# Optimization experiments

Measured on AMD Instinct MI355X. Metric: run time of the kernel, lower is better.

Reference implementation:

```python
import jax, jax.numpy as jnp
import numpy as np

D = 1024      # d_model
H = 16        # num_heads
HW = D // H   # head_width = 64
FF = 4 * D    # hidden_dim = 4096
BATCH = 2
T = 2048
EPS = 1e-5


def layer_norm(x, g, b):
    mu = jnp.mean(x, axis=-1, keepdims=True)
    var = jnp.mean(jnp.square(x - mu), axis=-1, keepdims=True)
    return (x - mu) * jax.lax.rsqrt(var + EPS) * g + b


def setup_inputs() -> dict:
    key = jax.random.key(0)
    ks = jax.random.split(key, 7)
    s = 0.02
    return {
        "x": jax.random.normal(ks[0], (BATCH, T, D), dtype=jnp.float32),
        "Wq": jax.random.normal(ks[1], (D, D), dtype=jnp.float32) * s,
        "Wk": jax.random.normal(ks[2], (D, D), dtype=jnp.float32) * s,
        "Wv": jax.random.normal(ks[3], (D, D), dtype=jnp.float32) * s,
        "W1": jax.random.normal(ks[4], (FF, D), dtype=jnp.float32) * s,
        "W2": jax.random.normal(ks[5], (D, FF), dtype=jnp.float32) * s,
        "g1": jnp.ones((D,), dtype=jnp.float32),
        "b1": jnp.zeros((D,), dtype=jnp.float32),
        "g2": jnp.ones((D,), dtype=jnp.float32),
        "b2": jnp.zeros((D,), dtype=jnp.float32),
    }


def reference(x, Wq, Wk, Wv, W1, W2, g1, b1, g2, b2):
    N, t, d = x.shape
    # norm1
    xn = layer_norm(x, g1, b1)

    # --- MHSA with ALiBi + causal mask (math mirrors torch module) ---
    def heads(y):  # (N,t,D) -> (N,H,t,HW)
        return y.reshape(N, t, H, HW).transpose(0, 2, 1, 3)

    q = heads(xn @ Wq.T)
    k = heads(xn @ Wk.T)
    v = heads(xn @ Wv.T)

    scores = jnp.einsum("nhqd,nhkd->nhqk", q, k) / np.sqrt(HW).astype(np.float32)

    pos = jnp.arange(t)
    rel = (pos[None, :] - pos[:, None]).astype(x.dtype)           # [t,t], rel[i,j]=j-i
    slopes = (2.0 ** (-(jnp.arange(1, H + 1)) * (8.0 / H))).astype(x.dtype)  # [H]
    alibi = slopes[:, None, None] * rel                            # [H,t,t]
    causal = jnp.where(pos[None, :] > pos[:, None],
                       jnp.array(-jnp.inf, x.dtype),
                       jnp.array(0.0, x.dtype))                    # [t,t]

    att = jax.nn.softmax(scores + alibi[None] + causal[None, None], axis=-1)
    o = jnp.einsum("nhqk,nhkd->nhqd", att, v)
    o = o.transpose(0, 2, 1, 3).reshape(N, t, d)

    att_out = xn + o

    # --- MLP: Linear -> SiLU -> Linear ---
    h = layer_norm(att_out, g2, b2)
    m = jax.nn.silu(h @ W1.T) @ W2.T
    return att_out + m
```

## Files before the change

kernel.cpp:

```cpp
#include <hip/hip_runtime.h>

#define DMODEL 1024
#define NHEAD  16
#define HWID   64
#define FFDIM  4096
#define NBATCH 2
#define SEQT   2048
#define NTOK   4096
#define QKLD   3072

using bf8    = __attribute__((ext_vector_type(8))) short;
using f32x4  = __attribute__((ext_vector_type(4))) float;
using f32x16 = __attribute__((ext_vector_type(16))) float;

__device__ inline short to_bf16(float f) {
  unsigned u = __float_as_uint(f);
  return (short)((u + 0x7fffu + ((u >> 16) & 1u)) >> 16);
}
__device__ inline float from_bf16(short s) {
  return __uint_as_float(((unsigned)(unsigned short)s) << 16);
}
__device__ inline float exp2_fast(float x) {
  float r;
  asm("v_exp_f32 %0, %1" : "=v"(r) : "v"(x));
  return r;
}
__device__ inline unsigned cvt_pk_bf16(float lo, float hi) {
  unsigned r;
  asm("v_cvt_pk_bf16_f32 %0, %1, %2" : "=v"(r) : "v"(lo), "v"(hi));
  return r;
}
__device__ inline void lds_load16(const void* g, void* l) {
  __builtin_amdgcn_global_load_lds(
      (const __attribute__((address_space(1))) void*)g,
      (__attribute__((address_space(3))) void*)l, 16, 0, 0);
}

__global__ __launch_bounds__(256)
void prep_kernel(const float* __restrict__ Wq, const float* __restrict__ Wk,
                 const float* __restrict__ Wv, const float* __restrict__ W1,
                 const float* __restrict__ W2, short* __restrict__ wqkv,
                 short* __restrict__ w1b, short* __restrict__ w2b,
                 const float* __restrict__ x, const float* __restrict__ g1,
                 const float* __restrict__ b1, short* __restrict__ xn) {
  __shared__ float red[8];
  if (blockIdx.x < 11264) {
    int i = blockIdx.x * 256 + threadIdx.x;
    const float* src;
    short* dst;
    if (i < 1048576)      { src = W1; dst = w1b; }
    else if (i < 2097152) { src = W2; dst = w2b;            i -= 1048576; }
    else if (i < 2359296) { src = Wq; dst = wqkv;           i -= 2097152; }
    else if (i < 2621440) { src = Wk; dst = wqkv + 1048576; i -= 2359296; }
    else                  { src = Wv; dst = wqkv + 2097152; i -= 2621440; }
    float4 v = ((const float4*)src)[i];
    short4 o;
    o.x = to_bf16(v.x); o.y = to_bf16(v.y);
    o.z = to_bf16(v.z); o.w = to_bf16(v.w);
    ((short4*)dst)[i] = o;
  } else {
    const int row = blockIdx.x - 11264;
    const int t = threadIdx.x;
    const float4 v = ((const float4*)(x + (long)row * DMODEL))[t];
    float s  = v.x + v.y + v.z + v.w;
    float s2 = v.x * v.x + v.y * v.y + v.z * v.z + v.w * v.w;
#pragma unroll
    for (int m = 1; m < 64; m <<= 1) {
      s  += __shfl_xor(s, m);
      s2 += __shfl_xor(s2, m);
    }
    if ((t & 63) == 0) { red[t >> 6] = s; red[4 + (t >> 6)] = s2; }
    __syncthreads();
    s  = red[0] + red[1] + red[2] + red[3];
    s2 = red[4] + red[5] + red[6] + red[7];
    const float mu = s * (1.f / DMODEL);
    const float rs = rsqrtf(s2 * (1.f / DMODEL) - mu * mu + 1e-5f);
    const float4 gv = ((const float4*)g1)[t];
    const float4 bv = ((const float4*)b1)[t];
    short4 o;
    o.x = to_bf16((v.x - mu) * rs * gv.x + bv.x);
    o.y = to_bf16((v.y - mu) * rs * gv.y + bv.y);
    o.z = to_bf16((v.z - mu) * rs * gv.z + bv.z);
    o.w = to_bf16((v.w - mu) * rs * gv.w + bv.w);
    ((short4*)(xn + (long)row * DMODEL))[t] = o;
  }
}

__global__ __launch_bounds__(256)
void ln_kernel(const float* __restrict__ x, const float* __restrict__ g,
               const float* __restrict__ b, short* __restrict__ out) {
  const int row = blockIdx.x;
  const int t = threadIdx.x;
  const float4 v = ((const float4*)(x + (long)row * DMODEL))[t];
  float s  = v.x + v.y + v.z + v.w;
  float s2 = v.x * v.x + v.y * v.y + v.z * v.z + v.w * v.w;
#pragma unroll
  for (int m = 1; m < 64; m <<= 1) {
    s  += __shfl_xor(s, m);
    s2 += __shfl_xor(s2, m);
  }
  __shared__ float red[8];
  if ((t & 63) == 0) { red[t >> 6] = s; red[4 + (t >> 6)] = s2; }
  __syncthreads();
  s  = red[0] + red[1] + red[2] + red[3];
  s2 = red[4] + red[5] + red[6] + red[7];
  const float mu = s * (1.f / DMODEL);
  const float rs = rsqrtf(s2 * (1.f / DMODEL) - mu * mu + 1e-5f);
  const float4 gv = ((const float4*)g)[t];
  const float4 bv = ((const float4*)b)[t];
  short4 o;
  o.x = to_bf16((v.x - mu) * rs * gv.x + bv.x);
  o.y = to_bf16((v.y - mu) * rs * gv.y + bv.y);
  o.z = to_bf16((v.z - mu) * rs * gv.z + bv.z);
  o.w = to_bf16((v.w - mu) * rs * gv.w + bv.w);
  ((short4*)(out + (long)row * DMODEL))[t] = o;
}

template <int EPI, int NF>
__global__ __launch_bounds__(512, 2)
void gemm256(const short* __restrict__ A, const short* __restrict__ Bw,
             void* __restrict__ Cout, int N, int lda, int ldb, int Kslice,
             long zstride) {
  __shared__ short lds[2][2][16384];
  const int tid = threadIdx.x;
  const int wid = tid >> 6, lane = tid & 63;
  const int l15 = lane & 15, l4 = lane >> 4;
  const int wm = wid >> 2, wn = wid & 3;
  const int BROWS = NF * 64;

  const int gx = gridDim.x, nwg = gx * gridDim.y;
  const int wg = blockIdx.y * gx + blockIdx.x;
  const int sw = (wg & 7) * (nwg >> 3) + (wg >> 3);
  const int sx = gx >> 2;
  const int st = sw >> 4, w16 = sw & 15;
  const long bm = (long)((st / sx) * 4 + (w16 >> 2)) * 256;
  const long bn = (long)((st % sx) * 4 + (w16 & 3)) * BROWS;
  const long kofs = (long)blockIdx.z * Kslice;
  const int NT = Kslice >> 6;

  long arow[2], brow[2];
  int  sgel[2], dofs[2];
#pragma unroll
  for (int l = 0; l < 2; ++l) {
    const int g = l * 512 + tid;
    const int row = g >> 2;
    sgel[l] = ((g & 3) ^ ((row >> 1) & 3)) * 8;
    dofs[l] = g * 16;
    arow[l] = (bm + row) * (long)lda + kofs;
    const int rb = (row < BROWS) ? row : (BROWS - 1);
    brow[l] = (bn + rb) * (long)ldb + kofs;
  }
  auto stage_half = [&](int h) {
    if (h >= (NT << 2)) return;
    const int th = h >> 2, hi = h & 3, buf = th & 1;
    const int ks = hi >> 1, isA = hi & 1;
    char* db = (char*)&lds[buf][isA ? 0 : 1][0] + ks * 16384;
    const long kb = (long)th * 64 + ks * 32;
#pragma unroll
    for (int l = 0; l < 2; ++l) {
      const short* src = (isA ? A + arow[l] : Bw + brow[l]) + kb + sgel[l];
      lds_load16(src, db + dofs[l]);
    }
  };

  const int xsw = (l4 ^ ((l15 >> 1) & 3)) << 4;
  const int aofs = (wm * 128 + l15) * 64 + xsw;
  const int bofs = (wn * (NF * 16) + l15) * 64 + xsw;

  f32x4 acc[8][NF] = {};
  bf8 fa[4], fa2[4], fb[NF];

#define PH_MID                                             \
  __builtin_amdgcn_s_barrier();                            \
  __builtin_amdgcn_s_setprio(1);
#define PH_END                                             \
  __builtin_amdgcn_s_setprio(0);                           \
  __builtin_amdgcn_s_barrier();                            \
  asm volatile("" ::: "memory");

#pragma unroll
  for (int h = 0; h < 7; ++h) stage_half(h);
  asm volatile("s_waitcnt vmcnt(6)" ::: "memory");
  __builtin_amdgcn_s_barrier();
  asm volatile("" ::: "memory");

  for (int u = 0; u < NT; ++u) {
    const int buf = u & 1;
    const char* pa = (const char*)&lds[buf][0][0];
    const char* pb = (const char*)&lds[buf][1][0];
#pragma unroll
    for (int m = 0; m < 4; ++m) fa[m] = *(const bf8*)(pa + aofs + m * 1024);
#pragma unroll
    for (int n = 0; n < NF; ++n) fb[n] = *(const bf8*)(pb + bofs + n * 1024);
    stage_half(4 * u + 7);
    PH_MID
#pragma unroll
    for (int m = 0; m < 4; ++m)
#pragma unroll
      for (int n = 0; n < NF; ++n)
        acc[m][n] = __builtin_amdgcn_mfma_f32_16x16x32_bf16(fa[m], fb[n], acc[m][n], 0, 0, 0);
    PH_END
#pragma unroll
    for (int m = 0; m < 4; ++m) fa2[m] = *(const bf8*)(pa + aofs + (4 + m) * 1024);
    stage_half(4 * u + 8);
    PH_MID
#pragma unroll
    for (int m = 0; m < 4; ++m)
#pragma unroll
      for (int n = 0; n < NF; ++n)
        acc[4 + m][n] = __builtin_amdgcn_mfma_f32_16x16x32_bf16(fa2[m], fb[n], acc[4 + m][n], 0, 0, 0);
    PH_END
#pragma unroll
    for (int m = 0; m < 4; ++m) fa[m] = *(const bf8*)(pa + 16384 + aofs + m * 1024);
#pragma unroll
    for (int n = 0; n < NF; ++n) fb[n] = *(const bf8*)(pb + 16384 + bofs + n * 1024);
    stage_half(4 * u + 9);
    PH_MID
#pragma unroll
    for (int m = 0; m < 4; ++m)
#pragma unroll
      for (int n = 0; n < NF; ++n)
        acc[m][n] = __builtin_amdgcn_mfma_f32_16x16x32_bf16(fa[m], fb[n], acc[m][n], 0, 0, 0);
    PH_END
#pragma unroll
    for (int m = 0; m < 4; ++m) fa2[m] = *(const bf8*)(pa + 16384 + aofs + (4 + m) * 1024);
    stage_half(4 * u + 10);
    if (u <= NT - 3)      asm volatile("s_waitcnt vmcnt(6)" ::: "memory");
    else if (u == NT - 2) asm volatile("s_waitcnt vmcnt(0)" ::: "memory");
    PH_MID
#pragma unroll
    for (int m = 0; m < 4; ++m)
#pragma unroll
      for (int n = 0; n < NF; ++n)
        acc[4 + m][n] = __builtin_amdgcn_mfma_f32_16x16x32_bf16(fa2[m], fb[n], acc[4 + m][n], 0, 0, 0);
    PH_END
  }
#undef PH_MID
#undef PH_END

#pragma unroll
  for (int mg = 0; mg < 8; ++mg)
#pragma unroll
    for (int n = 0; n < NF; ++n) {
      const long col = bn + wn * (NF * 16) + n * 16 + l15;
#pragma unroll
      for (int r = 0; r < 4; ++r) {
        const long row = bm + wm * 128 + mg * 16 + l4 * 4 + r;
        float v = acc[mg][n][r];
        if (EPI == 0) {
          ((short*)Cout)[row * N + col] = to_bf16(v);
        } else if (EPI == 1) {
          ((short*)Cout)[row * N + col] = to_bf16(v / (1.f + __expf(-v)));
        } else {
          ((short*)Cout)[blockIdx.z * zstride + row * N + col] = to_bf16(v);
        }
      }
    }
}

__global__ __launch_bounds__(256)
void pack_kv(const short* __restrict__ qkv, short* __restrict__ Kp,
             short* __restrict__ Vp) {
  __shared__ short tile[64][72];
  const int bx = blockIdx.x, bh = blockIdx.y;
  const int b = bh >> 4, h = bh & 15;
  const int t = threadIdx.x;
  if (bx < 64) {
    const int g = bx;
    const int row = t >> 3, cc = t & 7, c = cc >> 1, hi = cc & 1;
    const bf8 v = *(const bf8*)&qkv[(long)(b * SEQT + g * 32 + row) * QKLD +
                                    1024 + h * HWID + c * 16 + hi * 8];
    *(bf8*)&Kp[(((long)bh * 256 + g * 4 + c) * 64 + hi * 32 + row) * 8] = v;
  } else {
    const int tc = bx - 64;
    {
      const int r = t >> 2, c = (t & 3) * 16;
      const long src = (long)(b * SEQT + tc * 64 + r) * QKLD + 2048 + h * HWID + c;
      *(bf8*)&tile[r][c]     = *(const bf8*)&qkv[src];
      *(bf8*)&tile[r][c + 8] = *(const bf8*)&qkv[src + 8];
    }
    __syncthreads();
    const int dg = t >> 7, ch = (t >> 5) & 3, row = t & 31;
#pragma unroll
    for (int hi = 0; hi < 2; ++hi) {
      short o[8];
#pragma unroll
      for (int j = 0; j < 8; ++j) o[j] = tile[ch * 16 + hi * 8 + j][dg * 32 + row];
      *(bf8*)&Vp[(((long)bh * 256 + dg * 128 + tc * 4 + ch) * 64 + hi * 32 + row) * 8] =
          *(bf8*)o;
    }
  }
}

__global__ __launch_bounds__(64, 2)
void attn_kernel(const short* __restrict__ qkv, const short* __restrict__ Kp,
                 const short* __restrict__ Vp, const short* __restrict__ xn,
                 float* __restrict__ att) {
  const int L = blockIdx.x;
  const int bh = (L & 7) * 4 + ((L >> 3) & 3);
  const int u = L >> 5;
  const int qtile = (u < 32) ? (63 - u) : (u - 32);
  const int b = bh >> 4, h = bh & 15;
  const int q0 = qtile * 32;
  const int lane = threadIdx.x;
  const int l31 = lane & 31, hi = lane >> 5;
  const long tokbase = (long)b * SEQT;

  bf8 qf[4];
  {
    const short* qrow = qkv + (tokbase + q0 + l31) * QKLD + h * HWID + hi * 8;
#pragma unroll
    for (int c = 0; c < 4; ++c) qf[c] = *(const bf8*)(qrow + c * 16);
  }

  const float slope2 = exp2f(-0.5f * (float)(h + 1)) * 1.44269504f;
  const float sc2 = 0.125f * 1.44269504f;
  float arr[16];
#pragma unroll
  for (int r = 0; r < 16; ++r) arr[r] = slope2 * (float)((r & 3) + 8 * (r >> 2));
  const float hofs = slope2 * 4.f * (float)hi;
  const float qabs = (float)(q0 + l31);

  float m2 = -1e30f, lsum = 0.f;
  f32x16 acc0 = {}, acc1 = {};
  const int ktm = q0 >> 6;
  const bf8* kfb = (const bf8*)Kp + (long)bh * 16384 + lane;
  const bf8* vfb = (const bf8*)Vp + (long)bh * 16384 + lane;

  bf8 kc[8], kn[8], vc[8];
#pragma unroll
  for (int c = 0; c < 4; ++c) {
    kc[c]     = kfb[c * 64];
    kc[4 + c] = kfb[256 + c * 64];
  }

#pragma unroll 2
  for (int kt = 0; kt <= ktm; ++kt) {
    const int k0 = kt * 64;
    const long vb = (long)kt * 256;
#pragma unroll
    for (int ch = 0; ch < 4; ++ch) {
      vc[ch]     = vfb[vb + ch * 64];
      vc[4 + ch] = vfb[8192 + vb + ch * 64];
    }
    const long nb = (long)(kt < ktm ? kt + 1 : kt) * 512;
#pragma unroll
    for (int c = 0; c < 4; ++c) {
      kn[c]     = kfb[nb + c * 64];
      kn[4 + c] = kfb[nb + 256 + c * 64];
    }
    f32x16 s0 = {}, s1 = {};
#pragma unroll
    for (int c = 0; c < 4; ++c) {
      s0 = __builtin_amdgcn_mfma_f32_32x32x16_bf16(kc[c], qf[c], s0, 0, 0, 0);
      s1 = __builtin_amdgcn_mfma_f32_32x32x16_bf16(kc[4 + c], qf[c], s1, 0, 0, 0);
    }
    const float base = slope2 * ((float)k0 - qabs) + hofs;
    float s[32];
#pragma unroll
    for (int r = 0; r < 16; ++r) {
      s[r]      = fmaf(s0[r], sc2, base + arr[r]);
      s[16 + r] = fmaf(s1[r], sc2, base + arr[r] + slope2 * 32.f);
    }
    if (kt == ktm) {
      const int qi = q0 + l31;
#pragma unroll
      for (int r = 0; r < 16; ++r) {
        const int krel = (r & 3) + 8 * (r >> 2) + 4 * hi;
        if (k0 + krel > qi)      s[r]      = -1e30f;
        if (k0 + 32 + krel > qi) s[16 + r] = -1e30f;
      }
    }
    float ma = s[0], mb = s[1], mc = s[2], md = s[3];
#pragma unroll
    for (int i = 4; i < 32; i += 4) {
      ma = fmaxf(ma, s[i]); mb = fmaxf(mb, s[i + 1]);
      mc = fmaxf(mc, s[i + 2]); md = fmaxf(md, s[i + 3]);
    }
    float pm = fmaxf(fmaxf(ma, mb), fmaxf(mc, md));
    pm = fmaxf(pm, __shfl_xor(pm, 32));
    if (!__all(pm - m2 <= 11.0f)) {
      const float nm = fmaxf(m2, pm);
      const float alpha = exp2_fast(m2 - nm);
      m2 = nm;
      lsum *= alpha;
      acc0 *= alpha;
      acc1 *= alpha;
    }
    float p[32];
#pragma unroll
    for (int i = 0; i < 32; ++i) p[i] = exp2_fast(s[i] - m2);
    float sa = p[0], sb = p[1], sc = p[2], sd = p[3];
#pragma unroll
    for (int i = 4; i < 32; i += 4) {
      sa += p[i]; sb += p[i + 1]; sc += p[i + 2]; sd += p[i + 3];
    }
    float rs = (sa + sb) + (sc + sd);
    rs += __shfl_xor(rs, 32);
    lsum += rs;
    unsigned cpk[16];
#pragma unroll
    for (int g = 0; g < 8; ++g) {
      cpk[g]     = cvt_pk_bf16(p[2 * g], p[2 * g + 1]);
      cpk[8 + g] = cvt_pk_bf16(p[16 + 2 * g], p[16 + 2 * g + 1]);
    }
    bf8 pb[4];
#pragma unroll
    for (int ch = 0; ch < 4; ++ch) {
      const int cb = (ch >> 1) * 8 + (ch & 1) * 4;
      unsigned u0 = cpk[cb + 0], u2 = cpk[cb + 2];
      unsigned u1 = cpk[cb + 1], u3 = cpk[cb + 3];
      asm("v_permlane32_swap_b32 %0, %1" : "+v"(u0), "+v"(u2));
      asm("v_permlane32_swap_b32 %0, %1" : "+v"(u1), "+v"(u3));
      union { unsigned u[4]; bf8 v; } f;
      f.u[0] = u0; f.u[1] = u1; f.u[2] = u2; f.u[3] = u3;
      pb[ch] = f.v;
    }
#pragma unroll
    for (int ch = 0; ch < 4; ++ch) {
      acc0 = __builtin_amdgcn_mfma_f32_32x32x16_bf16(vc[ch], pb[ch], acc0, 0, 0, 0);
      acc1 = __builtin_amdgcn_mfma_f32_32x32x16_bf16(vc[4 + ch], pb[ch], acc1, 0, 0, 0);
    }
#pragma unroll
    for (int i = 0; i < 8; ++i) kc[i] = kn[i];
  }

  __shared__ float Os[32 * 68];
  const float rl = 1.f / lsum;
#pragma unroll
  for (int r = 0; r < 16; ++r) {
    const int d0 = (r & 3) + 8 * (r >> 2) + 4 * hi;
    Os[l31 * 68 + d0]      = acc0[r] * rl;
    Os[l31 * 68 + 32 + d0] = acc1[r] * rl;
  }
  __syncthreads();
#pragma unroll
  for (int it = 0; it < 8; ++it) {
    const int idx = it * 64 + lane;
    const int row = idx >> 4, c4 = idx & 15;
    const float4 ov = *(const float4*)&Os[row * 68 + c4 * 4];
    const long gbase = (tokbase + q0 + row) * DMODEL + h * HWID + c4 * 4;
    const short4 xv = *(const short4*)&xn[gbase];
    float4 o;
    o.x = ov.x + from_bf16(xv.x);
    o.y = ov.y + from_bf16(xv.y);
    o.z = ov.z + from_bf16(xv.z);
    o.w = ov.w + from_bf16(xv.w);
    *(float4*)&att[gbase] = o;
  }
}

__global__ __launch_bounds__(256)
void combine_kernel(const short* __restrict__ p, float* __restrict__ dout, int n4) {
  int i = blockIdx.x * 256 + threadIdx.x;
  if (i < n4) {
    float4 a = ((const float4*)dout)[i];
    short4 b0 = ((const short4*)(p))[i];
    short4 b1 = ((const short4*)(p + 4194304))[i];
    short4 b2 = ((const short4*)(p + 8388608))[i];
    short4 b3 = ((const short4*)(p + 12582912))[i];
    a.x += (from_bf16(b0.x) + from_bf16(b1.x)) + (from_bf16(b2.x) + from_bf16(b3.x));
    a.y += (from_bf16(b0.y) + from_bf16(b1.y)) + (from_bf16(b2.y) + from_bf16(b3.y));
    a.z += (from_bf16(b0.z) + from_bf16(b1.z)) + (from_bf16(b2.z) + from_bf16(b3.z));
    a.w += (from_bf16(b0.w) + from_bf16(b1.w)) + (from_bf16(b2.w) + from_bf16(b3.w));
    ((float4*)dout)[i] = a;
  }
}

extern "C" void kernel_launch(void* const* d_in, const int* in_sizes, int n_in,
                              void* d_out, int out_size, void* d_ws, size_t ws_size,
                              hipStream_t stream) {
  (void)in_sizes; (void)n_in; (void)out_size; (void)ws_size;
  const float* x  = (const float*)d_in[0];
  const float* Wq = (const float*)d_in[1];
  const float* Wk = (const float*)d_in[2];
  const float* Wv = (const float*)d_in[3];
  const float* W1 = (const float*)d_in[4];
  const float* W2 = (const float*)d_in[5];
  const float* g1 = (const float*)d_in[6];
  const float* b1 = (const float*)d_in[7];
  const float* g2 = (const float*)d_in[8];
  const float* b2 = (const float*)d_in[9];

  char* ws = (char*)d_ws;
  const size_t MB = 1024 * 1024;
  short* wqkv_b = (short*)(ws + 0);
  short* w1_b   = (short*)(ws + 6  * MB);
  short* w2_b   = (short*)(ws + 14 * MB);
  short* xn     = (short*)(ws + 22 * MB);
  short* qkv    = (short*)(ws + 30 * MB);
  short* m1     = (short*)(ws + 22 * MB);
  short* Kp     = (short*)(ws + 54 * MB);
  short* Vp     = (short*)(ws + 62 * MB);
  short* hb     = (short*)(ws + 70 * MB);
  short* parts  = (short*)(ws + 54 * MB);
  float* att    = (float*)d_out;

  prep_kernel<<<15360, 256, 0, stream>>>(Wq, Wk, Wv, W1, W2, wqkv_b, w1_b, w2_b,
                                         x, g1, b1, xn);

  gemm256<0, 3><<<dim3(16, 16), 512, 0, stream>>>(xn, wqkv_b, qkv, QKLD, DMODEL,
                                                  DMODEL, DMODEL, 0);
  pack_kv<<<dim3(96, 32), 256, 0, stream>>>(qkv, Kp, Vp);

  attn_kernel<<<2048, 64, 0, stream>>>(qkv, Kp, Vp, xn, att);

  ln_kernel<<<NTOK, 256, 0, stream>>>(att, g2, b2, hb);

  gemm256<1, 4><<<dim3(16, 16), 512, 0, stream>>>(hb, w1_b, m1, FFDIM, DMODEL,
                                                  DMODEL, DMODEL, 0);
  gemm256<2, 4><<<dim3(4, 16, 4), 512, 0, stream>>>(m1, w2_b, parts, DMODEL, FFDIM,
                                                    FFDIM, 1024, (long)NTOK * DMODEL);
  combine_kernel<<<4096, 256, 0, stream>>>(parts, (float*)d_out, 1048576);
}
```

Before: 194.7 us.

## Process two query tiles per attention wave to share K/V loads

Each attention wavefront now handles 64 query rows, as two 32-row sub-tiles with separate softmax state and accumulators, instead of one 32-row tile. Each K/V block it loads feeds both sub-tiles, which halves K/V global traffic per query. The diagonal tile's causal mask is specialized per sub-tile. The grid is halved to 1024 single-wave blocks, so there are fewer waves to hide latency and more registers per wave, traded for more independent MFMA work inside each wave.

```diff
diff --git a/kernel.cpp b/kernel.cpp
--- a/kernel.cpp
+++ b/kernel.cpp
@@ -299,31 +299,31 @@
   const int L = blockIdx.x;
   const int bh = (L & 7) * 4 + ((L >> 3) & 3);
   const int u = L >> 5;
-  const int qtile = (u < 32) ? (63 - u) : (u - 32);
+  const int qp = (u < 16) ? (31 - u) : (u - 16);
   const int b = bh >> 4, h = bh & 15;
-  const int q0 = qtile * 32;
+  const int q0a = qp * 64;
   const int lane = threadIdx.x;
   const int l31 = lane & 31, hi = lane >> 5;
   const long tokbase = (long)b * SEQT;
 
-  bf8 qf[4];
+  bf8 qfA[4], qfB[4];
   {
-    const short* qrow = qkv + (tokbase + q0 + l31) * QKLD + h * HWID + hi * 8;
-#pragma unroll
-    for (int c = 0; c < 4; ++c) qf[c] = *(const bf8*)(qrow + c * 16);
+    const short* qra = qkv + (tokbase + q0a + l31) * QKLD + h * HWID + hi * 8;
+    const short* qrb = qra + 32 * QKLD;
+#pragma unroll
+    for (int c = 0; c < 4; ++c) {
+      qfA[c] = *(const bf8*)(qra + c * 16);
+      qfB[c] = *(const bf8*)(qrb + c * 16);
+    }
   }
 
   const float slope2 = exp2f(-0.5f * (float)(h + 1)) * 1.44269504f;
   const float sc2 = 0.125f * 1.44269504f;
-  float arr[16];
-#pragma unroll
-  for (int r = 0; r < 16; ++r) arr[r] = slope2 * (float)((r & 3) + 8 * (r >> 2));
   const float hofs = slope2 * 4.f * (float)hi;
-  const float qabs = (float)(q0 + l31);
-
-  float m2 = -1e30f, lsum = 0.f;
-  f32x16 acc0 = {}, acc1 = {};
-  const int ktm = q0 >> 6;
+
+  float m2a = -1e30f, lsa = 0.f, m2b = -1e30f, lsb = 0.f;
+  f32x16 accA0 = {}, accA1 = {}, accB0 = {}, accB1 = {};
+  const int ktm = qp;
   const bf8* kfb = (const bf8*)Kp + (long)bh * 16384 + lane;
   const bf8* vfb = (const bf8*)Vp + (long)bh * 16384 + lane;
 
@@ -334,48 +334,41 @@
     kc[4 + c] = kfb[256 + c * 64];
   }
 
-#pragma unroll 2
-  for (int kt = 0; kt <= ktm; ++kt) {
-    const int k0 = kt * 64;
-    const long vb = (long)kt * 256;
-#pragma unroll
-    for (int ch = 0; ch < 4; ++ch) {
-      vc[ch]     = vfb[vb + ch * 64];
-      vc[4 + ch] = vfb[8192 + vb + ch * 64];
-    }
-    const long nb = (long)(kt < ktm ? kt + 1 : kt) * 512;
+  auto run_tile = [&](const bf8 (&qf)[4], int q0t, int k0, int diag,
+                      float& m2, float& lsum, f32x16& A0, f32x16& A1) {
+    f32x16 s0v = {}, s1v = {};
 #pragma unroll
     for (int c = 0; c < 4; ++c) {
-      kn[c]     = kfb[nb + c * 64];
-      kn[4 + c] = kfb[nb + 256 + c * 64];
-    }
-    f32x16 s0 = {}, s1 = {};
-#pragma unroll
-    for (int c = 0; c < 4; ++c) {
-      s0 = __builtin_amdgcn_mfma_f32_32x32x16_bf16(kc[c], qf[c], s0, 0, 0, 0);
-      s1 = __builtin_amdgcn_mfma_f32_32x32x16_bf16(kc[4 + c], qf[c], s1, 0, 0, 0);
-    }
-    const float base = slope2 * ((float)k0 - qabs) + hofs;
+      s0v = __builtin_amdgcn_mfma_f32_32x32x16_bf16(kc[c], qf[c], s0v, 0, 0, 0);
+      s1v = __builtin_amdgcn_mfma_f32_32x32x16_bf16(kc[4 + c], qf[c], s1v, 0, 0, 0);
+    }
+    const float base = slope2 * ((float)k0 - (float)(q0t + l31)) + hofs;
     float s[32];
 #pragma unroll
     for (int r = 0; r < 16; ++r) {
-      s[r]      = fmaf(s0[r], sc2, base + arr[r]);
-      s[16 + r] = fmaf(s1[r], sc2, base + arr[r] + slope2 * 32.f);
-    }
-    if (kt == ktm) {
-      const int qi = q0 + l31;
+      const float ar = fmaf(slope2, (float)((r & 3) + 8 * (r >> 2)), base);
+      s[r]      = fmaf(s0v[r], sc2, ar);
+      s[16 + r] = fmaf(s1v[r], sc2, ar + slope2 * 32.f);
+    }
+    if (diag == 1) {
 #pragma unroll
       for (int r = 0; r < 16; ++r) {
         const int krel = (r & 3) + 8 * (r >> 2) + 4 * hi;
-        if (k0 + krel > qi)      s[r]      = -1e30f;
-        if (k0 + 32 + krel > qi) s[16 + r] = -1e30f;
+        if (krel > l31) s[r] = -1e30f;
+        s[16 + r] = -1e30f;
       }
+    } else if (diag == 2) {
+#pragma unroll
+      for (int r = 0; r < 16; ++r) {
+        const int krel = (r & 3) + 8 * (r >> 2) + 4 * hi;
+        if (krel > l31) s[16 + r] = -1e30f;
+      }
     }
     float ma = s[0], mb = s[1], mc = s[2], md = s[3];
 #pragma unroll
-    for (int i = 4; i < 32; i += 4) {
-      ma = fmaxf(ma, s[i]); mb = fmaxf(mb, s[i + 1]);
-      mc = fmaxf(mc, s[i + 2]); md = fmaxf(md, s[i + 3]);
+    for (int i2 = 4; i2 < 32; i2 += 4) {
+      ma = fmaxf(ma, s[i2]); mb = fmaxf(mb, s[i2 + 1]);
+      mc = fmaxf(mc, s[i2 + 2]); md = fmaxf(md, s[i2 + 3]);
     }
     float pm = fmaxf(fmaxf(ma, mb), fmaxf(mc, md));
     pm = fmaxf(pm, __shfl_xor(pm, 32));
@@ -384,70 +377,85 @@
       const float alpha = exp2_fast(m2 - nm);
       m2 = nm;
       lsum *= alpha;
-      acc0 *= alpha;
-      acc1 *= alpha;
+      A0 *= alpha;
+      A1 *= alpha;
     }
     float p[32];
 #pragma unroll
-    for (int i = 0; i < 32; ++i) p[i] = exp2_fast(s[i] - m2);
+    for (int i2 = 0; i2 < 32; ++i2) p[i2] = exp2_fast(s[i2] - m2);
     float sa = p[0], sb = p[1], sc = p[2], sd = p[3];
 #pragma unroll
-    for (int i = 4; i < 32; i += 4) {
-      sa += p[i]; sb += p[i + 1]; sc += p[i + 2]; sd += p[i + 3];
+    for (int i2 = 4; i2 < 32; i2 += 4) {
+      sa += p[i2]; sb += p[i2 + 1]; sc += p[i2 + 2]; sd += p[i2 + 3];
     }
     float rs = (sa + sb) + (sc + sd);
     rs += __shfl_xor(rs, 32);
     lsum += rs;
-    unsigned cpk[16];
-#pragma unroll
-    for (int g = 0; g < 8; ++g) {
-      cpk[g]     = cvt_pk_bf16(p[2 * g], p[2 * g + 1]);
-      cpk[8 + g] = cvt_pk_bf16(p[16 + 2 * g], p[16 + 2 * g + 1]);
-    }
-    bf8 pb[4];
 #pragma unroll
     for (int ch = 0; ch < 4; ++ch) {
-      const int cb = (ch >> 1) * 8 + (ch & 1) * 4;
-      unsigned u0 = cpk[cb + 0], u2 = cpk[cb + 2];
-      unsigned u1 = cpk[cb + 1], u3 = cpk[cb + 3];
+      const int bp = ch * 8;
+      unsigned u0 = cvt_pk_bf16(p[bp],     p[bp + 1]);
+      unsigned u1 = cvt_pk_bf16(p[bp + 2], p[bp + 3]);
+      unsigned u2 = cvt_pk_bf16(p[bp + 4], p[bp + 5]);
+      unsigned u3 = cvt_pk_bf16(p[bp + 6], p[bp + 7]);
       asm("v_permlane32_swap_b32 %0, %1" : "+v"(u0), "+v"(u2));
       asm("v_permlane32_swap_b32 %0, %1" : "+v"(u1), "+v"(u3));
-      union { unsigned u[4]; bf8 v; } f;
-      f.u[0] = u0; f.u[1] = u1; f.u[2] = u2; f.u[3] = u3;
-      pb[ch] = f.v;
-    }
+      union { unsigned uu[4]; bf8 v; } f;
+      f.uu[0] = u0; f.uu[1] = u1; f.uu[2] = u2; f.uu[3] = u3;
+      A0 = __builtin_amdgcn_mfma_f32_32x32x16_bf16(vc[ch], f.v, A0, 0, 0, 0);
+      A1 = __builtin_amdgcn_mfma_f32_32x32x16_bf16(vc[4 + ch], f.v, A1, 0, 0, 0);
+    }
+  };
+
+#pragma unroll 2
+  for (int kt = 0; kt <= ktm; ++kt) {
+    const int k0 = kt * 64;
+    const long vb = (long)kt * 256;
 #pragma unroll
     for (int ch = 0; ch < 4; ++ch) {
-      acc0 = __builtin_amdgcn_mfma_f32_32x32x16_bf16(vc[ch], pb[ch], acc0, 0, 0, 0);
-      acc1 = __builtin_amdgcn_mfma_f32_32x32x16_bf16(vc[4 + ch], pb[ch], acc1, 0, 0, 0);
-    }
-#pragma unroll
-    for (int i = 0; i < 8; ++i) kc[i] = kn[i];
+      vc[ch]     = vfb[vb + ch * 64];
+      vc[4 + ch] = vfb[8192 + vb + ch * 64];
+    }
+    const long nb = (long)(kt < ktm ? kt + 1 : kt) * 512;
+#pragma unroll
+    for (int c = 0; c < 4; ++c) {
+      kn[c]     = kfb[nb + c * 64];
+      kn[4 + c] = kfb[nb + 256 + c * 64];
+    }
+    const bool dg = (kt == ktm);
+    run_tile(qfA, q0a,      k0, dg ? 1 : 0, m2a, lsa, accA0, accA1);
+    run_tile(qfB, q0a + 32, k0, dg ? 2 : 0, m2b, lsb, accB0, accB1);
+#pragma unroll
+    for (int i2 = 0; i2 < 8; ++i2) kc[i2] = kn[i2];
   }
 
   __shared__ float Os[32 * 68];
-  const float rl = 1.f / lsum;
-#pragma unroll
-  for (int r = 0; r < 16; ++r) {
-    const int d0 = (r & 3) + 8 * (r >> 2) + 4 * hi;
-    Os[l31 * 68 + d0]      = acc0[r] * rl;
-    Os[l31 * 68 + 32 + d0] = acc1[r] * rl;
-  }
+  auto epi = [&](const f32x16& A0, const f32x16& A1, float lsum, int q0t) {
+    const float rl = 1.f / lsum;
+#pragma unroll
+    for (int r = 0; r < 16; ++r) {
+      const int d0 = (r & 3) + 8 * (r >> 2) + 4 * hi;
+      Os[l31 * 68 + d0]      = A0[r] * rl;
+      Os[l31 * 68 + 32 + d0] = A1[r] * rl;
+    }
+#pragma unroll
+    for (int it = 0; it < 8; ++it) {
+      const int idx = it * 64 + lane;
+      const int row = idx >> 4, c4 = idx & 15;
+      const float4 ov = *(const float4*)&Os[row * 68 + c4 * 4];
+      const long gbase = (tokbase + q0t + row) * DMODEL + h * HWID + c4 * 4;
+      const short4 xv = *(const short4*)&xn[gbase];
+      float4 o;
+      o.x = ov.x + from_bf16(xv.x);
+      o.y = ov.y + from_bf16(xv.y);
+      o.z = ov.z + from_bf16(xv.z);
+      o.w = ov.w + from_bf16(xv.w);
+      *(float4*)&att[gbase] = o;
+    }
+  };
+  epi(accA0, accA1, lsa, q0a);
   __syncthreads();
-#pragma unroll
-  for (int it = 0; it < 8; ++it) {
-    const int idx = it * 64 + lane;
-    const int row = idx >> 4, c4 = idx & 15;
-    const float4 ov = *(const float4*)&Os[row * 68 + c4 * 4];
-    const long gbase = (tokbase + q0 + row) * DMODEL + h * HWID + c4 * 4;
-    const short4 xv = *(const short4*)&xn[gbase];
-    float4 o;
-    o.x = ov.x + from_bf16(xv.x);
-    o.y = ov.y + from_bf16(xv.y);
-    o.z = ov.z + from_bf16(xv.z);
-    o.w = ov.w + from_bf16(xv.w);
-    *(float4*)&att[gbase] = o;
-  }
+  epi(accB0, accB1, lsb, q0a + 32);
 }
 
 __global__ __launch_bounds__(256)
@@ -503,7 +511,7 @@
                                                   DMODEL, DMODEL, 0);
   pack_kv<<<dim3(96, 32), 256, 0, stream>>>(qkv, Kp, Vp);
 
-  attn_kernel<<<2048, 64, 0, stream>>>(qkv, Kp, Vp, xn, att);
+  attn_kernel<<<1024, 64, 0, stream>>>(qkv, Kp, Vp, xn, att);
 
   ln_kernel<<<NTOK, 256, 0, stream>>>(att, g2, b2, hb);
 
```

After: 206.0 us. 1.06x slower.
